# Performance work log

Measured on AMD Instinct MI355X. Metric: run time of the kernel, lower is better.

Reference implementation:

```python
import jax, jax.numpy as jnp
import numpy as np

D_MODEL = 256
NUM_HEADS = 8
HEAD_DIM = D_MODEL // NUM_HEADS
WS = 7
BN_EPS = 1e-5


def setup_inputs() -> dict:
    key = jax.random.key(0)
    ks = jax.random.split(key, 5)
    B, C, H, W = 4, D_MODEL, 224, 224
    s = 1.0 / np.sqrt(C)
    return {
        "x": jax.random.normal(ks[0], (B, C, H, W), jnp.float32),
        "Wq": jax.random.normal(ks[1], (C, C), jnp.float32) * s,
        "Wk": jax.random.normal(ks[2], (C, C), jnp.float32) * s,
        "Wv": jax.random.normal(ks[3], (C, C), jnp.float32) * s,
        "Wo": jax.random.normal(ks[4], (C, C), jnp.float32) * s,
        "gamma": jnp.ones((C,), jnp.float32),
        "beta": jnp.zeros((C,), jnp.float32),
    }


def _to_windows(t, B, nh, hd, nHw, nWw):
    # t: (B, C, Hp, Wp) -> (B, nh, nWin, ws*ws, hd)
    t = t.reshape(B, nh, hd, nHw, WS, nWw, WS)
    t = t.transpose(0, 1, 3, 5, 4, 6, 2)  # (B, nh, nHw, nWw, ws, ws, hd)
    return t.reshape(B, nh, nHw * nWw, WS * WS, hd)


def reference(x, Wq, Wk, Wv, Wo, gamma, beta):
    B, C, H, W = x.shape
    pad_h = (-H) % WS
    pad_w = (-W) % WS
    q = jnp.einsum('oc,bchw->bohw', Wq, x)
    k = jnp.einsum('oc,bchw->bohw', Wk, x)
    v = jnpp = jnp.einsum('oc,bchw->bohw', Wv, x)
    if pad_h or pad_w:
        pad = ((0, 0), (0, 0), (0, pad_h), (0, pad_w))
        q, k, v = jnp.pad(q, pad), jnp.pad(k, pad), jnp.pad(v, pad)
    Hp, Wp = H + pad_h, W + pad_w
    nHw, nWw = Hp // WS, Wp // WS
    q_w = _to_windows(q, B, NUM_HEADS, HEAD_DIM, nHw, nWw)
    k_w = _to_windows(k, B, NUM_HEADS, HEAD_DIM, nHw, nWw)
    v_w = _to_windows(v, B, NUM_HEADS, HEAD_DIM, nHw, nWw)
    scale = 1.0 / np.sqrt(HEAD_DIM)
    attn = jnp.einsum('bhnqd,bhnkd->bhnqk', q_w, k_w) * scale
    attn = jax.nn.softmax(attn, axis=-1)
    out_w = jnp.einsum('bhnqk,bhnkd->bhnqd', attn, v_w)
    # fold windows back: (B, nh, nWin, ws*ws, hd) -> (B, C, Hp, Wp)
    out = out_w.reshape(B, NUM_HEADS, nHw, nWw, WS, WS, HEAD_DIM)
    out = out.transpose(0, 1, 6, 2, 4, 3, 5).reshape(B, C, Hp, Wp)
    out = out[:, :, :H, :W]
    out = jnp.einsum('oc,bchw->bohw', Wo, out)
    y = x + out
    # BatchNorm2d (training-mode batch statistics, biased variance)
    mean = jnp.mean(y, axis=(0, 2, 3), keepdims=True)
    var = jnp.mean((y - mean) ** 2, axis=(0, 2, 3), keepdims=True)
    yhat = (y - mean) * jax.lax.rsqrt(var + BN_EPS)
    return yhat * gamma[None, :, None, None] + beta[None, :, None, None]
```

## Files before the change

### kernel.cpp

```cpp
#include <hip/hip_runtime.h>
#include <stdint.h>

typedef __attribute__((ext_vector_type(8))) short short8;
typedef __attribute__((ext_vector_type(4))) float f32x4;

#define MFMA16(a,b,c) __builtin_amdgcn_mfma_f32_16x16x32_bf16((a),(b),(c),0,0,0)

#define GLL16(g, l) __builtin_amdgcn_global_load_lds( \
    (const __attribute__((address_space(1))) void*)(g), \
    (__attribute__((address_space(3))) void*)(l), 16, 0, 0)

__device__ __forceinline__ unsigned short f2bf(float f){
  unsigned u = __builtin_bit_cast(unsigned, f);
  u += 0x7fffu + ((u >> 16) & 1u);
  return (unsigned short)(u >> 16);
}
__device__ __forceinline__ float bf2f(unsigned short s){
  unsigned u = ((unsigned)s) << 16;
  return __builtin_bit_cast(float, u);
}

static constexpr int HW_ = 50176;

__device__ __forceinline__ int panel_off(int r, int c64){
  return r * 64 + ((((c64 >> 3) ^ (r & 7))) << 3) + (c64 & 7);
}

__global__ __launch_bounds__(256) void k_convw(const float* __restrict__ Wq, const float* __restrict__ Wk,
                        const float* __restrict__ Wv, const float* __restrict__ Wo,
                        unsigned short* __restrict__ Wf, unsigned short* __restrict__ Wob){
  int gid = blockIdx.x * 256 + threadIdx.x;
  if (gid < 24576){
    int lane = gid & 63;
    int r1 = gid >> 6;
    int t = r1 % 6;
    int r2 = r1 / 6;
    int kq = r2 & 7, hh = r2 >> 3;
    const float* W = (t < 2) ? Wq : (t < 4) ? Wk : Wv;
    int ch = hh * 32 + (t & 1) * 16 + (lane & 15);
    int k0 = kq * 32 + (lane >> 4) * 8;
    const float* src = W + ch * 256 + k0;
    float4 a = *(const float4*)src, b2 = *(const float4*)(src + 4);
    short8 v;
    v[0]=f2bf(a.x); v[1]=f2bf(a.y); v[2]=f2bf(a.z); v[3]=f2bf(a.w);
    v[4]=f2bf(b2.x); v[5]=f2bf(b2.y); v[6]=f2bf(b2.z); v[7]=f2bf(b2.w);
    *(short8*)(Wf + (size_t)gid * 8) = v;
  } else {
    int og = gid - 24576;
    int o = og >> 5, ck = og & 31;
    const float* src = Wo + o * 256 + ck * 8;
    float4 a = *(const float4*)src, b2 = *(const float4*)(src + 4);
    short8 v;
    v[0]=f2bf(a.x); v[1]=f2bf(a.y); v[2]=f2bf(a.z); v[3]=f2bf(a.w);
    v[4]=f2bf(b2.x); v[5]=f2bf(b2.y); v[6]=f2bf(b2.z); v[7]=f2bf(b2.w);
    int kq = ck >> 3;
    int off = panel_off(o & 127, (ck & 7) * 8);
    *(short8*)(Wob + ((o >> 7) * 4 + kq) * 8192 + off) = v;
  }
}

__global__ __launch_bounds__(256) void k_xw(const float* __restrict__ x, unsigned short* __restrict__ xw){
  int bid = blockIdx.x;
  int cq = bid & 15, wh = (bid >> 4) & 31, b = bid >> 9;
  __shared__ __align__(16) unsigned short tile[25088];
  int tid = threadIdx.x;
  for (int it = 0; it < 25; ++it){
    int idx = it * 256 + tid;
    if (idx < 6272){
      int c = idx & 15;
      int t2 = idx >> 4;
      int r = t2 / 56;
      int w4 = t2 % 56;
      float4 v = *(const float4*)(x + ((size_t)(b * 256 + cq * 16 + c)) * HW_ + (wh * 7 + r) * 224 + w4 * 4);
      float vv[4] = {v.x, v.y, v.z, v.w};
      int w0 = w4 * 4;
      int ww = w0 / 7;
      int cl = w0 % 7;
#pragma unroll
      for (int i = 0; i < 4; ++i){
        int px = r * 7 + cl;
        tile[ww * 784 + px * 16 + (((c >> 3) ^ (px & 1)) << 3) + (c & 7)] = f2bf(vv[i]);
        if (++cl == 7){ cl = 0; ++ww; }
      }
    }
  }
  __syncthreads();
  size_t wb = ((size_t)(b * 1024 + wh * 32)) * 16384;
  for (int it = 0; it < 13; ++it){
    int id = it * 256 + tid;
    if (id < 3136){
      int ww = id / 98;
      int rem = id - ww * 98;
      int px = rem >> 1, half = rem & 1;
      short8 v = *(const short8*)(tile + ww * 784 + px * 16 + ((half ^ (px & 1)) << 3));
      int cc = cq * 2 + half;
      int pos = (cc & 24) | ((cc ^ px) & 7);
      *(short8*)(xw + wb + (size_t)ww * 16384 + px * 256 + pos * 8) = v;
    }
  }
}

__global__ __launch_bounds__(512, 2) void k_fused(const unsigned short* __restrict__ xw,
                                                  const unsigned short* __restrict__ Wf,
                                                  unsigned short* __restrict__ attnP){
  int bid = blockIdx.x;
  int wg = (bid & 7) * 512 + (bid >> 3);
  int b = wg >> 10;
  int win = wg & 1023;
  int wh = win >> 5, ww = win & 31;
  int tid = threadIdx.x;
  int lane = tid & 63;
  int h = tid >> 6;

  __shared__ __align__(16) unsigned short lds[65536];

  {
    if (tid < 448){
      int rr = 50 + (tid >> 5), ch = tid & 31;
      short8 z = {};
      *(short8*)(lds + 49152 + rr * 256 + ch * 8) = z;
    }
    const unsigned short* xwin = xw + ((size_t)(b * 1024 + wh * 32 + ww)) * 16384;
#pragma unroll
    for (int c3 = 0; c3 < 3; ++c3){
      int k = c3 * 8 + h;
      int row = 2 * k + (lane >> 5);
      GLL16(xwin + row * 256 + (lane & 31) * 8, lds + 49152 + k * 512);
    }
    if (h == 0)
      GLL16(xwin + 48 * 256 + (lane & 31) * 8, lds + 49152 + 24 * 512);
  }
  __syncthreads();

  f32x4 aq[4][2] = {}, ak[4][2] = {}, av[2][4] = {};
  for (int kq = 0; kq < 8; ++kq){
    short8 xf[4];
#pragma unroll
    for (int pt = 0; pt < 4; ++pt){
      int px = pt * 16 + (lane & 15);
      int chk = (kq * 4 + (lane >> 4)) ^ (px & 7);
      xf[pt] = *(const short8*)(lds + 49152 + px * 256 + chk * 8);
    }
    short8 wfr[6];
#pragma unroll
    for (int t = 0; t < 6; ++t)
      wfr[t] = *(const short8*)(Wf + ((size_t)((h * 8 + kq) * 6 + t) * 64 + lane) * 8);
#pragma unroll
    for (int pt = 0; pt < 4; ++pt){
      aq[pt][0] = MFMA16(xf[pt], wfr[0], aq[pt][0]);
      aq[pt][1] = MFMA16(xf[pt], wfr[1], aq[pt][1]);
      ak[pt][0] = MFMA16(xf[pt], wfr[2], ak[pt][0]);
      ak[pt][1] = MFMA16(xf[pt], wfr[3], ak[pt][1]);
      av[0][pt] = MFMA16(wfr[4], xf[pt], av[0][pt]);
      av[1][pt] = MFMA16(wfr[5], xf[pt], av[1][pt]);
    }
  }
#pragma unroll
  for (int pt = 0; pt < 4; ++pt)
#pragma unroll
    for (int t = 0; t < 2; ++t)
#pragma unroll
      for (int j = 0; j < 4; ++j){
        int px = pt * 16 + (lane >> 4) * 4 + j;
        int ch = h * 32 + t * 16 + (lane & 15);
        int pos = px * 256 + (((ch >> 3) ^ (px & 7)) << 3) + (ch & 7);
        lds[pos]         = f2bf(aq[pt][t][j]);
        lds[16384 + pos] = f2bf(ak[pt][t][j]);
      }
#pragma unroll
  for (int ct = 0; ct < 2; ++ct)
#pragma unroll
    for (int pt = 0; pt < 4; ++pt)
#pragma unroll
      for (int j = 0; j < 4; ++j){
        int ch = h * 32 + ct * 16 + (lane >> 4) * 4 + j;
        int px = pt * 16 + (lane & 15);
        lds[32768 + ch * 64 + (((px >> 3) ^ (ch & 7)) << 3) + (px & 7)] = f2bf(av[ct][pt][j]);
      }
  __syncthreads();

  short8 kf[4], qf[4];
#pragma unroll
  for (int i = 0; i < 4; ++i){
    int px = i * 16 + (lane & 15);
    int chk = (h * 4 + (lane >> 4)) ^ (px & 7);
    qf[i] = *(const short8*)(lds + px * 256 + chk * 8);
    kf[i] = *(const short8*)(lds + 16384 + px * 256 + chk * 8);
  }
  f32x4 s[4][4] = {};
#pragma unroll
  for (int mi = 0; mi < 4; ++mi)
#pragma unroll
    for (int ni = 0; ni < 4; ++ni)
      s[mi][ni] = MFMA16(kf[mi], qf[ni], s[mi][ni]);
  __syncthreads();

  const float cexp = 0.25504437f;
  unsigned short* sP = lds + h * 4096;
#pragma unroll
  for (int ni = 0; ni < 4; ++ni){
    float m = -3.0e38f;
#pragma unroll
    for (int mi = 0; mi < 4; ++mi)
#pragma unroll
      for (int r = 0; r < 4; ++r){
        int kp = mi * 16 + ((lane >> 4) * 4) + r;
        if (kp < 49) m = fmaxf(m, s[mi][ni][r]);
      }
    m = fmaxf(m, __shfl_xor(m, 16));
    m = fmaxf(m, __shfl_xor(m, 32));
    float sum = 0.f;
    float pv[4][4];
#pragma unroll
    for (int mi = 0; mi < 4; ++mi)
#pragma unroll
      for (int r = 0; r < 4; ++r){
        int kp = mi * 16 + ((lane >> 4) * 4) + r;
        float e2 = (kp < 49) ? exp2f((s[mi][ni][r] - m) * cexp) : 0.f;
        pv[mi][r] = e2; sum += e2;
      }
    sum += __shfl_xor(sum, 16);
    sum += __shfl_xor(sum, 32);
    float inv = 1.0f / sum;
    int q = ni * 16 + (lane & 15);
#pragma unroll
    for (int mi = 0; mi < 4; ++mi)
#pragma unroll
      for (int r = 0; r < 4; ++r){
        int kp = mi * 16 + ((lane >> 4) * 4) + r;
        int bo = (q * 128 + kp * 2) ^ ((q & 7) << 4);
        sP[bo >> 1] = f2bf(pv[mi][r] * inv);
      }
  }

  f32x4 o[4][2] = {};
#pragma unroll
  for (int kc = 0; kc < 2; ++kc){
    short8 pa[4], vb[2];
#pragma unroll
    for (int mtp = 0; mtp < 4; ++mtp){
      int row = mtp * 16 + (lane & 15);
      int bo = (row * 128 + kc * 64 + (lane >> 4) * 16) ^ ((row & 7) << 4);
      pa[mtp] = *(const short8*)(sP + (bo >> 1));
    }
#pragma unroll
    for (int ntp = 0; ntp < 2; ++ntp){
      int ch = h * 32 + ntp * 16 + (lane & 15);
      int k0 = kc * 32 + (lane >> 4) * 8;
      vb[ntp] = *(const short8*)(lds + 32768 + ch * 64 + (((k0 >> 3) ^ (ch & 7)) << 3));
    }
#pragma unroll
    for (int mtp = 0; mtp < 4; ++mtp)
#pragma unroll
      for (int ntp = 0; ntp < 2; ++ntp)
        o[mtp][ntp] = MFMA16(pa[mtp], vb[ntp], o[mtp][ntp]);
  }
#pragma unroll
  for (int mtp = 0; mtp < 4; ++mtp)
#pragma unroll
    for (int ntp = 0; ntp < 2; ++ntp)
#pragma unroll
      for (int r = 0; r < 4; ++r){
        int px = mtp * 16 + (lane >> 4) * 4 + r;
        int ch = h * 32 + ntp * 16 + (lane & 15);
        lds[49152 + px * 256 + (((ch >> 3) ^ (px & 7)) << 3) + (ch & 7)] = f2bf(o[mtp][ntp][r]);
      }
  __syncthreads();

  size_t pb0 = (size_t)b * 392 * 4;
#pragma unroll
  for (int it = 0; it < 4; ++it){
    int id = it * 512 + tid;
    int px = id >> 5, ck = id & 31;
    if (px < 49){
      short8 v = *(const short8*)(lds + 49152 + px * 256 + ((ck ^ (px & 7)) << 3));
      int pg = (wh * 7 + px / 7) * 224 + ww * 7 + px % 7;
      int nt = pg >> 7, pr = pg & 127;
      size_t off = (pb0 + (size_t)nt * 4 + (ck >> 3)) * 8192 + panel_off(pr, (ck & 7) * 8);
      *(short8*)(attnP + off) = v;
    }
  }
}

__global__ __launch_bounds__(256) void k_gemm_out(const unsigned short* __restrict__ Wp,
                                                  const unsigned short* __restrict__ Bp,
                                                  const float* __restrict__ x,
                                                  unsigned short* __restrict__ ybf,
                                                  float* __restrict__ partials){
  int bid = blockIdx.x;
  int wg = (bid & 7) * 392 + (bid >> 3);
  int mt = wg & 1; int rest = wg >> 1;
  int nt = rest % 392; int b = rest / 392;

  __shared__ __align__(16) unsigned short lds[32768];

  int tid = threadIdx.x;
  int lane = tid & 63;
  int wave = tid >> 6;
  int wm = wave >> 1, wn = wave & 1;

  const unsigned short* Apan = Wp + (size_t)mt * 4 * 8192;
  const unsigned short* Bpan = Bp + ((size_t)(b * 392 + nt)) * 4 * 8192;

  int aoff[2][4], boff[2][4];
#pragma unroll
  for (int kk = 0; kk < 2; ++kk)
#pragma unroll
    for (int i = 0; i < 4; ++i){
      int rowA = wm * 64 + i * 16 + (lane & 15);
      aoff[kk][i] = rowA * 64 + (((kk * 4 + (lane >> 4)) ^ (rowA & 7)) << 3);
      int rowB = wn * 64 + i * 16 + (lane & 15);
      boff[kk][i] = rowB * 64 + (((kk * 4 + (lane >> 4)) ^ (rowB & 7)) << 3);
    }
  int cb = wave * 2048;
  f32x4 acc[4][4] = {};

#pragma unroll
  for (int j = 0; j < 4; ++j){
    int o2 = cb + j * 512;
    GLL16(Apan + o2 + lane * 8, lds + o2);
    GLL16(Bpan + o2 + lane * 8, lds + 8192 + o2);
  }
  __syncthreads();

  int cur = 0;
  for (int kq = 0; kq < 4; ++kq){
    if (kq < 3){
      const unsigned short* Ak = Apan + (kq + 1) * 8192;
      const unsigned short* Bk = Bpan + (kq + 1) * 8192;
      unsigned short* dst = lds + (cur ^ 1) * 16384;
#pragma unroll
      for (int j = 0; j < 4; ++j){
        int o2 = cb + j * 512;
        GLL16(Ak + o2 + lane * 8, dst + o2);
        GLL16(Bk + o2 + lane * 8, dst + 8192 + o2);
      }
    }
    const unsigned short* Alds = lds + cur * 16384;
    const unsigned short* Blds = Alds + 8192;
#pragma unroll
    for (int kk = 0; kk < 2; ++kk){
      short8 af[4], bfv[4];
#pragma unroll
      for (int i = 0; i < 4; ++i) af[i]  = *(const short8*)(Alds + aoff[kk][i]);
#pragma unroll
      for (int j = 0; j < 4; ++j) bfv[j] = *(const short8*)(Blds + boff[kk][j]);
#pragma unroll
      for (int i = 0; i < 4; ++i)
#pragma unroll
        for (int j = 0; j < 4; ++j)
          acc[i][j] = MFMA16(af[i], bfv[j], acc[i][j]);
    }
    __syncthreads();
    cur ^= 1;
  }
  float ps[4][4] = {}, pq[4][4] = {};
#pragma unroll
  for (int i = 0; i < 4; ++i)
#pragma unroll
    for (int j = 0; j < 4; ++j){
      int o = mt * 128 + wm * 64 + i * 16 + (lane >> 4) * 4;
      int p = nt * 128 + wn * 64 + j * 16 + (lane & 15);
      size_t base = ((size_t)(b * 256 + o)) * HW_ + p;
#pragma unroll
      for (int r2 = 0; r2 < 4; ++r2){
        float v = acc[i][j][r2] + x[base + (size_t)r2 * HW_];
        ybf[base + (size_t)r2 * HW_] = f2bf(v);
        ps[i][r2] += v;
        pq[i][r2] += v * v;
      }
    }
  float* fl = (float*)lds;
#pragma unroll
  for (int i = 0; i < 4; ++i)
#pragma unroll
    for (int r2 = 0; r2 < 4; ++r2){
      float a = ps[i][r2], q2 = pq[i][r2];
      a += __shfl_xor(a, 1);  q2 += __shfl_xor(q2, 1);
      a += __shfl_xor(a, 2);  q2 += __shfl_xor(q2, 2);
      a += __shfl_xor(a, 4);  q2 += __shfl_xor(q2, 4);
      a += __shfl_xor(a, 8);  q2 += __shfl_xor(q2, 8);
      if ((lane & 15) == 0){
        int cl = wm * 64 + i * 16 + (lane >> 4) * 4 + r2;
        fl[wn * 128 + cl] = a;
        fl[256 + wn * 128 + cl] = q2;
      }
    }
  __syncthreads();
  if (tid < 128){
    partials[(size_t)wg * 256 + tid]       = fl[tid] + fl[128 + tid];
    partials[(size_t)wg * 256 + 128 + tid] = fl[256 + tid] + fl[384 + tid];
  }
}

__global__ __launch_bounds__(256) void k_stats2(const float* __restrict__ partials, float* __restrict__ stats){
  int c = blockIdx.x;
  int mt = c >> 7, cl = c & 127;
  int t = threadIdx.x;
  float s = 0.f, q = 0.f;
  for (int idx = t; idx < 1568; idx += 256){
    const float* p = partials + (size_t)(2 * idx + mt) * 256;
    s += p[cl]; q += p[128 + cl];
  }
  __shared__ float r1[256], r2[256];
  r1[t] = s; r2[t] = q; __syncthreads();
  for (int off = 128; off > 0; off >>= 1){
    if (t < off){ r1[t] += r1[t + off]; r2[t] += r2[t + off]; }
    __syncthreads();
  }
  if (t == 0){
    float mean = r1[0] * (1.f / 200704.f);
    float var  = r2[0] * (1.f / 200704.f) - mean * mean;
    stats[c] = mean;
    stats[256 + c] = rsqrtf(var + 1e-5f);
  }
}

__global__ __launch_bounds__(256) void k_norm(const unsigned short* __restrict__ ybf,
                                              const float* __restrict__ stats,
                                              const float* __restrict__ gamma, const float* __restrict__ beta,
                                              float* __restrict__ out){
  const long long total = 6422528LL;
  for (long long idx = (long long)blockIdx.x * 256 + threadIdx.x; idx < total; idx += (long long)gridDim.x * 256){
    int c = (int)((idx / 6272) & 255);
    float sc = stats[256 + c] * gamma[c];
    float sh = beta[c] - stats[c] * sc;
    short8 v = *(const short8*)(ybf + idx * 8);
    float4 o0, o1;
    o0.x = bf2f((unsigned short)v[0]) * sc + sh;
    o0.y = bf2f((unsigned short)v[1]) * sc + sh;
    o0.z = bf2f((unsigned short)v[2]) * sc + sh;
    o0.w = bf2f((unsigned short)v[3]) * sc + sh;
    o1.x = bf2f((unsigned short)v[4]) * sc + sh;
    o1.y = bf2f((unsigned short)v[5]) * sc + sh;
    o1.z = bf2f((unsigned short)v[6]) * sc + sh;
    o1.w = bf2f((unsigned short)v[7]) * sc + sh;
    *(float4*)(out + idx * 8)     = o0;
    *(float4*)(out + idx * 8 + 4) = o1;
  }
}

extern "C" void kernel_launch(void* const* d_in, const int* in_sizes, int n_in,
                              void* d_out, int out_size, void* d_ws, size_t ws_size,
                              hipStream_t stream){
  const float* x     = (const float*)d_in[0];
  const float* Wq    = (const float*)d_in[1];
  const float* Wk    = (const float*)d_in[2];
  const float* Wv    = (const float*)d_in[3];
  const float* Wo    = (const float*)d_in[4];
  const float* gamma = (const float*)d_in[5];
  const float* beta  = (const float*)d_in[6];
  float* out = (float*)d_out;

  char* ws = (char*)d_ws;
  unsigned short* Wf     = (unsigned short*)ws;
  unsigned short* Wo_b   = (unsigned short*)(ws + 393216);
  float*          stats  = (float*)(ws + 524288);
  unsigned short* xw     = (unsigned short*)(ws + 1048576);
  unsigned short* attnP  = (unsigned short*)(ws + 1048576 + 134217728);
  float*          partials = (float*)(ws + 1048576 + 134217728 + 102760448);
  unsigned short* ybf    = xw;

  k_convw<<<128, 256, 0, stream>>>(Wq, Wk, Wv, Wo, Wf, Wo_b);
  k_xw<<<2048, 256, 0, stream>>>(x, xw);
  k_fused<<<4096, 512, 0, stream>>>(xw, Wf, attnP);
  k_gemm_out<<<3136, 256, 0, stream>>>(Wo_b, attnP, x, ybf, partials);
  k_stats2<<<256, 256, 0, stream>>>(partials, stats);
  k_norm<<<4096, 256, 0, stream>>>(ybf, stats, gamma, beta, out);
}
```

Measured before the change: 503.1 us.

## Split fused window-attention block into two half-head blocks with smaller LDS

```diff
diff --git a/kernel.cpp b/kernel.cpp
--- a/kernel.cpp
+++ b/kernel.cpp
@@ -91,70 +91,82 @@
     if (id < 3136){
       int ww = id / 98;
       int rem = id - ww * 98;
-      int px = rem >> 1, half = rem & 1;
-      short8 v = *(const short8*)(tile + ww * 784 + px * 16 + ((half ^ (px & 1)) << 3));
-      int cc = cq * 2 + half;
-      int pos = (cc & 24) | ((cc ^ px) & 7);
-      *(short8*)(xw + wb + (size_t)ww * 16384 + px * 256 + pos * 8) = v;
-    }
-  }
-}
-
-__global__ __launch_bounds__(512, 2) void k_fused(const unsigned short* __restrict__ xw,
+      int px = rem >> 1, hb = rem & 1;
+      short8 v = *(const short8*)(tile + ww * 784 + px * 16 + ((hb ^ (px & 1)) << 3));
+      int cc = cq * 2 + hb;
+      int half = cc >> 4, c4 = cc & 15;
+      int pos = (c4 & 8) | ((c4 ^ px) & 7);
+      *(short8*)(xw + wb + (size_t)ww * 16384 + half * 8192 + px * 128 + pos * 8) = v;
+    }
+  }
+}
+
+__global__ __launch_bounds__(256, 3) void k_fused(const unsigned short* __restrict__ xw,
                                                   const unsigned short* __restrict__ Wf,
                                                   unsigned short* __restrict__ attnP){
   int bid = blockIdx.x;
-  int wg = (bid & 7) * 512 + (bid >> 3);
-  int b = wg >> 10;
-  int win = wg & 1023;
-  int wh = win >> 5, ww = win & 31;
+  int wg = (bid & 7) * 1024 + (bid >> 3);
+  int hh = wg & 1; int win = wg >> 1;
+  int b = win >> 10;
+  int wh = (win >> 5) & 31, ww = win & 31;
   int tid = threadIdx.x;
   int lane = tid & 63;
-  int h = tid >> 6;
-
-  __shared__ __align__(16) unsigned short lds[65536];
-
-  {
-    if (tid < 448){
-      int rr = 50 + (tid >> 5), ch = tid & 31;
-      short8 z = {};
-      *(short8*)(lds + 49152 + rr * 256 + ch * 8) = z;
-    }
-    const unsigned short* xwin = xw + ((size_t)(b * 1024 + wh * 32 + ww)) * 16384;
-#pragma unroll
-    for (int c3 = 0; c3 < 3; ++c3){
-      int k = c3 * 8 + h;
-      int row = 2 * k + (lane >> 5);
-      GLL16(xwin + row * 256 + (lane & 31) * 8, lds + 49152 + k * 512);
-    }
-    if (h == 0)
-      GLL16(xwin + 48 * 256 + (lane & 31) * 8, lds + 49152 + 24 * 512);
+  int hl = tid >> 6;
+  int hg = hh * 4 + hl;
+
+  __shared__ __align__(16) unsigned short lds[24576];
+
+  const unsigned short* xwin = xw + (size_t)win * 16384;
+
+  if (tid < 240){
+    int rr = 49 + (tid >> 4), ck = tid & 15;
+    short8 z = {};
+    *(short8*)(lds + rr * 128 + ck * 8) = z;
+  }
+#pragma unroll
+  for (int it = 0; it < 4; ++it){
+    int chunk = it * 256 + tid;
+    if (chunk < 784) GLL16(xwin + chunk * 8, lds + chunk * 8);
   }
   __syncthreads();
 
   f32x4 aq[4][2] = {}, ak[4][2] = {}, av[2][4] = {};
-  for (int kq = 0; kq < 8; ++kq){
-    short8 xf[4];
-#pragma unroll
-    for (int pt = 0; pt < 4; ++pt){
-      int px = pt * 16 + (lane & 15);
-      int chk = (kq * 4 + (lane >> 4)) ^ (px & 7);
-      xf[pt] = *(const short8*)(lds + 49152 + px * 256 + chk * 8);
-    }
-    short8 wfr[6];
-#pragma unroll
-    for (int t = 0; t < 6; ++t)
-      wfr[t] = *(const short8*)(Wf + ((size_t)((h * 8 + kq) * 6 + t) * 64 + lane) * 8);
-#pragma unroll
-    for (int pt = 0; pt < 4; ++pt){
-      aq[pt][0] = MFMA16(xf[pt], wfr[0], aq[pt][0]);
-      aq[pt][1] = MFMA16(xf[pt], wfr[1], aq[pt][1]);
-      ak[pt][0] = MFMA16(xf[pt], wfr[2], ak[pt][0]);
-      ak[pt][1] = MFMA16(xf[pt], wfr[3], ak[pt][1]);
-      av[0][pt] = MFMA16(wfr[4], xf[pt], av[0][pt]);
-      av[1][pt] = MFMA16(wfr[5], xf[pt], av[1][pt]);
-    }
-  }
+  for (int half = 0; half < 2; ++half){
+    for (int kq = 0; kq < 4; ++kq){
+      short8 xf[4];
+#pragma unroll
+      for (int pt = 0; pt < 4; ++pt){
+        int px = pt * 16 + (lane & 15);
+        int c = kq * 4 + (lane >> 4);
+        int cs = (c & 8) | ((c ^ px) & 7);
+        xf[pt] = *(const short8*)(lds + px * 128 + cs * 8);
+      }
+      short8 wfr[6];
+      int kqg = half * 4 + kq;
+#pragma unroll
+      for (int t = 0; t < 6; ++t)
+        wfr[t] = *(const short8*)(Wf + ((size_t)((hg * 8 + kqg) * 6 + t) * 64 + lane) * 8);
+#pragma unroll
+      for (int pt = 0; pt < 4; ++pt){
+        aq[pt][0] = MFMA16(xf[pt], wfr[0], aq[pt][0]);
+        aq[pt][1] = MFMA16(xf[pt], wfr[1], aq[pt][1]);
+        ak[pt][0] = MFMA16(xf[pt], wfr[2], ak[pt][0]);
+        ak[pt][1] = MFMA16(xf[pt], wfr[3], ak[pt][1]);
+        av[0][pt] = MFMA16(wfr[4], xf[pt], av[0][pt]);
+        av[1][pt] = MFMA16(wfr[5], xf[pt], av[1][pt]);
+      }
+    }
+    if (half == 0){
+      __syncthreads();
+#pragma unroll
+      for (int it = 0; it < 4; ++it){
+        int chunk = it * 256 + tid;
+        if (chunk < 784) GLL16(xwin + 8192 + chunk * 8, lds + chunk * 8);
+      }
+      __syncthreads();
+    }
+  }
+
 #pragma unroll
   for (int pt = 0; pt < 4; ++pt)
 #pragma unroll
@@ -162,30 +174,32 @@
 #pragma unroll
       for (int j = 0; j < 4; ++j){
         int px = pt * 16 + (lane >> 4) * 4 + j;
-        int ch = h * 32 + t * 16 + (lane & 15);
-        int pos = px * 256 + (((ch >> 3) ^ (px & 7)) << 3) + (ch & 7);
-        lds[pos]         = f2bf(aq[pt][t][j]);
+        int chl = hl * 32 + t * 16 + (lane & 15);
+        int ck = chl >> 3;
+        int pos = px * 128 + (((ck & 8) | ((ck ^ px) & 7)) << 3) + (chl & 7);
+        lds[8192 + pos]  = f2bf(aq[pt][t][j]);
         lds[16384 + pos] = f2bf(ak[pt][t][j]);
       }
+  __syncthreads();
 #pragma unroll
   for (int ct = 0; ct < 2; ++ct)
 #pragma unroll
     for (int pt = 0; pt < 4; ++pt)
 #pragma unroll
       for (int j = 0; j < 4; ++j){
-        int ch = h * 32 + ct * 16 + (lane >> 4) * 4 + j;
+        int chl = hl * 32 + ct * 16 + (lane >> 4) * 4 + j;
         int px = pt * 16 + (lane & 15);
-        lds[32768 + ch * 64 + (((px >> 3) ^ (ch & 7)) << 3) + (px & 7)] = f2bf(av[ct][pt][j]);
-      }
-  __syncthreads();
+        lds[chl * 64 + (((px >> 3) ^ (chl & 7)) << 3) + (px & 7)] = f2bf(av[ct][pt][j]);
+      }
 
   short8 kf[4], qf[4];
 #pragma unroll
   for (int i = 0; i < 4; ++i){
     int px = i * 16 + (lane & 15);
-    int chk = (h * 4 + (lane >> 4)) ^ (px & 7);
-    qf[i] = *(const short8*)(lds + px * 256 + chk * 8);
-    kf[i] = *(const short8*)(lds + 16384 + px * 256 + chk * 8);
+    int c = hl * 4 + (lane >> 4);
+    int cs = (c & 8) | ((c ^ px) & 7);
+    qf[i] = *(const short8*)(lds + 8192 + px * 128 + cs * 8);
+    kf[i] = *(const short8*)(lds + 16384 + px * 128 + cs * 8);
   }
   f32x4 s[4][4] = {};
 #pragma unroll
@@ -196,7 +210,7 @@
   __syncthreads();
 
   const float cexp = 0.25504437f;
-  unsigned short* sP = lds + h * 4096;
+  unsigned short* sP = lds + 8192 + hl * 4096;
 #pragma unroll
   for (int ni = 0; ni < 4; ++ni){
     float m = -3.0e38f;
@@ -245,9 +259,9 @@
     }
 #pragma unroll
     for (int ntp = 0; ntp < 2; ++ntp){
-      int ch = h * 32 + ntp * 16 + (lane & 15);
+      int chl = hl * 32 + ntp * 16 + (lane & 15);
       int k0 = kc * 32 + (lane >> 4) * 8;
-      vb[ntp] = *(const short8*)(lds + 32768 + ch * 64 + (((k0 >> 3) ^ (ch & 7)) << 3));
+      vb[ntp] = *(const short8*)(lds + chl * 64 + (((k0 >> 3) ^ (chl & 7)) << 3));
     }
 #pragma unroll
     for (int mtp = 0; mtp < 4; ++mtp)
@@ -262,21 +276,24 @@
 #pragma unroll
       for (int r = 0; r < 4; ++r){
         int px = mtp * 16 + (lane >> 4) * 4 + r;
-        int ch = h * 32 + ntp * 16 + (lane & 15);
-        lds[49152 + px * 256 + (((ch >> 3) ^ (px & 7)) << 3) + (ch & 7)] = f2bf(o[mtp][ntp][r]);
+        int ch5 = ntp * 16 + (lane & 15);
+        int c2 = ch5 >> 3;
+        sP[px * 32 + (((c2 ^ px) & 3) << 3) + (ch5 & 7)] = f2bf(o[mtp][ntp][r]);
       }
   __syncthreads();
 
   size_t pb0 = (size_t)b * 392 * 4;
 #pragma unroll
   for (int it = 0; it < 4; ++it){
-    int id = it * 512 + tid;
-    int px = id >> 5, ck = id & 31;
+    int id = it * 256 + tid;
+    int px = id >> 4, ck = id & 15;
     if (px < 49){
-      short8 v = *(const short8*)(lds + 49152 + px * 256 + ((ck ^ (px & 7)) << 3));
+      int hl2 = ck >> 2, c2 = ck & 3;
+      short8 v = *(const short8*)(lds + 8192 + hl2 * 4096 + px * 32 + (((c2 ^ px) & 3) << 3));
+      int ch0 = (hh * 4 + hl2) * 32 + c2 * 8;
       int pg = (wh * 7 + px / 7) * 224 + ww * 7 + px % 7;
       int nt = pg >> 7, pr = pg & 127;
-      size_t off = (pb0 + (size_t)nt * 4 + (ck >> 3)) * 8192 + panel_off(pr, (ck & 7) * 8);
+      size_t off = (pb0 + (size_t)nt * 4 + (ch0 >> 6)) * 8192 + panel_off(pr, ch0 & 63);
       *(short8*)(attnP + off) = v;
     }
   }
@@ -463,7 +480,7 @@
 
   k_convw<<<128, 256, 0, stream>>>(Wq, Wk, Wv, Wo, Wf, Wo_b);
   k_xw<<<2048, 256, 0, stream>>>(x, xw);
-  k_fused<<<4096, 512, 0, stream>>>(xw, Wf, attnP);
+  k_fused<<<8192, 256, 0, stream>>>(xw, Wf, attnP);
   k_gemm_out<<<3136, 256, 0, stream>>>(Wo_b, attnP, x, ybf, partials);
   k_stats2<<<256, 256, 0, stream>>>(partials, stats);
   k_norm<<<4096, 256, 0, stream>>>(ybf, stats, gamma, beta, out);
```

Result: faster. 487.3 us (-3.1%).
